# Performance work log

Hardware: AMD Instinct MI355X
Metric: run time of the kernel (lower is better)

## Reference

```python
import jax, jax.numpy as jnp
import numpy as np

TAU = 2.0       # LIF time constant
ALPHA = 4.0     # spikingjelly Sigmoid surrogate alpha
EPS = 1e-5      # BatchNorm eps
NUM_HEADS = 8

@jax.custom_vjp
def _spike(x):
    return (x >= 0.0).astype(x.dtype)

def _spike_fwd(x):
    return _spike(x), x

def _spike_bwd(x, g):
    s = jax.nn.sigmoid(ALPHA * x)
    return (g * ALPHA * s * (1.0 - s),)

_spike.defvjp(_spike_fwd, _spike_bwd)

def lif(x, v_th=1.0):
    """Multi-step LIF over leading time axis. v <- v + (x - v)/tau; hard reset to 0.
    detach_reset=True: spike in reset path is stop-gradient'ed."""
    def step(v, xt):
        v = v + (xt - v) / TAU
        s = _spike(v - v_th)
        v = v * (1.0 - jax.lax.stop_gradient(s))
        return v, s
    _, out = jax.lax.scan(step, jnp.zeros_like(x[0]), x)
    return out

def conv_bn(x, w, gamma, beta, mean, var, bias=None):
    """1x1 Conv1d over channel dim + BatchNorm1d (inference-style, running stats).
    x: [T,B,C,N], w: [Cout,Cin]."""
    y = jnp.einsum('tbcn,dc->tbdn', x, w)
    if bias is not None:
        y = y + bias[None, None, :, None]
    inv = gamma * jax.lax.rsqrt(var + EPS)
    return (y - mean[None, None, :, None]) * inv[None, None, :, None] + beta[None, None, :, None]

def _bn_params(key, C):
    k1, k2, k3 = jax.random.split(key, 3)
    gamma = 1.0 + 0.1 * jax.random.normal(k1, (C,), jnp.float32)
    beta = 0.1 * jax.random.normal(k2, (C,), jnp.float32)
    mean = 0.1 * jax.random.normal(k3, (C,), jnp.float32)
    var = jnp.ones((C,), jnp.float32)
    return gamma, beta, mean, var

def setup_inputs() -> dict:
    key = jax.random.key(0)
    ks = jax.random.split(key, 10)
    T, B, C, N = 4, 8, 512, 1024
    scale = 1.0 / np.sqrt(C)
    d = {}
    d['q'] = jax.random.normal(ks[0], (T, B, C, N), jnp.float32)
    d['k'] = jax.random.normal(ks[1], (T, B, C, N), jnp.float32)
    d['q_w'] = jax.random.normal(ks[2], (C, C), jnp.float32) * scale
    d['k_w'] = jax.random.normal(ks[3], (C, C), jnp.float32) * scale
    d['proj_w'] = jax.random.normal(ks[4], (C, C), jnp.float32) * scale
    d['proj_b'] = 0.01 * jax.random.normal(ks[5], (C,), jnp.float32)
    d['q_gamma'], d['q_beta'], d['q_mean'], d['q_var'] = _bn_params(ks[6], C)
    d['k_gamma'], d['k_beta'], d['k_mean'], d['k_var'] = _bn_params(ks[7], C)
    d['proj_gamma'], d['proj_beta'], d['proj_mean'], d['proj_var'] = _bn_params(ks[8], C)
    return d

def reference(q, k, q_w, k_w, proj_w, proj_b,
              q_gamma, q_beta, q_mean, q_var,
              k_gamma, k_beta, k_mean, k_var,
              proj_gamma, proj_beta, proj_mean, proj_var):
    T, B, C, N = q.shape
    H = NUM_HEADS
    Dh = C // H
    # Q path: conv1x1 + BN + LIF spikes, split heads
    q_s = lif(conv_bn(q, q_w, q_gamma, q_beta, q_mean, q_var))          # [T,B,C,N]
    q_h = q_s.reshape(T, B, H, Dh, N)
    # K path
    k_s = lif(conv_bn(k, k_w, k_gamma, k_beta, k_mean, k_var))          # [T,B,C,N]
    k_h = k_s.reshape(T, B, H, Dh, N)
    # Sum-pool Q over head_dim, spike-gate (threshold 0.5), multiply into K
    q_sum = jnp.sum(q_h, axis=3, keepdims=True)                         # [T,B,H,1,N]
    attn = lif(q_sum, v_th=0.5)                                         # [T,B,H,1,N]
    x = (attn * k_h).reshape(T, B, C, N)
    # Projection: conv1x1 (with bias) + BN + LIF
    x = conv_bn(x, proj_w, proj_gamma, proj_beta, proj_mean, proj_var, bias=proj_b)
    return lif(x)
```

## Files before the change

kernel.cpp:

```cpp
#include <hip/hip_runtime.h>
#include <hip/hip_fp16.h>
#include <stdint.h>

#define TT 4
#define BB 8
#define CC 512
#define NN 1024
#define HH 8

typedef unsigned char u8;
typedef _Float16 f16x8 __attribute__((ext_vector_type(8)));
typedef float f32x16 __attribute__((ext_vector_type(16)));

#define WF_BYTES ((size_t)2*64*512*16)
#define SZ_SPIKE ((size_t)TT*BB*CC*NN)
#define SZ_GATE  ((size_t)TT*BB*HH*NN)

union U4H { uint4 u; f16x8 v; };
__device__ __forceinline__ f16x8 ash(uint4 u){ U4H x; x.u = u; return x.v; }

#define MFMA_F16(a,b,c) __builtin_amdgcn_mfma_f32_32x32x16_f16((a),(b),(c),0,0,0)

__device__ __forceinline__ void gld_lds4(const void* g, void* l){
  __builtin_amdgcn_global_load_lds((const __attribute__((address_space(1))) void*)g,
                                   (__attribute__((address_space(3))) void*)l, 4, 0, 0);
}

#define WAITVM(N) asm volatile("s_waitcnt vmcnt(" #N ")" ::: "memory")
#define WAITLGKM0 asm volatile("s_waitcnt lgkmcnt(0)" ::: "memory")
#define SBAR() __builtin_amdgcn_s_barrier()
#define VMFENCE() asm volatile("" ::: "memory")

__device__ __forceinline__ void split16(float xs, uint32_t& h, uint32_t& m){
  __half hh = __float2half(xs);
  float hf = __half2float(hh);
  __half mm = __float2half(xs - hf);
  h = __half_as_ushort(hh);
  m = __half_as_ushort(mm);
}

__global__ __launch_bounds__(256)
void k_prep(const float* __restrict__ W0, const float* __restrict__ W1,
            const float* __restrict__ W2,
            u8* __restrict__ D0, u8* __restrict__ D1, u8* __restrict__ D2)
{
  const int which = blockIdx.y;
  const float* W = (which == 0) ? W0 : (which == 1) ? W1 : W2;
  u8* D = (which == 0) ? D0 : (which == 1) ? D1 : D2;
  const int tg  = blockIdx.x * 256 + threadIdx.x;
  const int row = tg >> 6;
  const int kh  = tg & 63;
  uint32_t Hw[4], Mw[4];
#pragma unroll
  for (int p = 0; p < 4; ++p){
    uint32_t h0, m0, h1, m1;
    split16(W[row * CC + kh * 8 + 2*p    ] * 64.0f, h0, m0);
    split16(W[row * CC + kh * 8 + 2*p + 1] * 64.0f, h1, m1);
    Hw[p] = h0 | (h1 << 16);
    Mw[p] = m0 | (m1 << 16);
  }
  *(uint4*)(D + ((size_t)(0*64 + kh)*512 + row) * 16) = make_uint4(Hw[0],Hw[1],Hw[2],Hw[3]);
  *(uint4*)(D + ((size_t)(1*64 + kh)*512 + row) * 16) = make_uint4(Mw[0],Mw[1],Mw[2],Mw[3]);
}

__global__ __launch_bounds__(512, 2)
void k_qk(const float* __restrict__ Q, const float* __restrict__ K,
          const u8* __restrict__ WFq, const u8* __restrict__ WFk,
          const float* __restrict__ qg, const float* __restrict__ qb,
          const float* __restrict__ qm, const float* __restrict__ qv,
          const float* __restrict__ kg, const float* __restrict__ kb,
          const float* __restrict__ km, const float* __restrict__ kv,
          u8* __restrict__ Sk, u8* __restrict__ Aa)
{
  __shared__ uint4 frag[2][1024];

  const int hw = blockIdx.x;
  const int lg = (hw & 7) * 64 + (hw >> 3);
  const int n0i  = lg & 31;
  const int b    = (lg >> 5) & 7;
  const int path = (lg >> 8) & 1;
  const int n0 = n0i << 5;
  const float* X = path ? K : Q;
  const u8* WF = path ? WFk : WFq;

  const int tid = threadIdx.x, lane = tid & 63, wid = tid >> 6;
  const int hi = lane >> 5, ln31 = lane & 31;

  const int c  = tid & 127;
  const int kq = tid >> 7;
  const int ct_t = c >> 5, nn = c & 31;
  const float* Xb = X + ((size_t)(ct_t*BB + b)*CC)*NN + n0 + nn;

  f32x16 acc[4][2];
#pragma unroll
  for (int i = 0; i < 4; ++i)
#pragma unroll
    for (int j = 0; j < 2; ++j)
#pragma unroll
      for (int r = 0; r < 16; ++r) acc[i][j][r] = 0.0f;

  uint4 A0[8], A1[8];
  float xr[8];

  auto loadX = [&](int tile){
    const float* xp = Xb + (size_t)(tile*32 + kq*8)*NN;
#pragma unroll
    for (int j = 0; j < 8; ++j) xr[j] = xp[(size_t)j*NN];
  };
  auto loadA = [&](int H, uint4* A){
#pragma unroll
    for (int s = 0; s < 2; ++s)
#pragma unroll
      for (int ksc = 0; ksc < 2; ++ksc)
#pragma unroll
        for (int rt = 0; rt < 2; ++rt)
          A[(s*2 + ksc)*2 + rt] = *(const uint4*)(WF +
              ((size_t)(s*64 + H*4 + ksc*2 + hi)*512
               + wid*64 + rt*32 + ln31) * 16);
  };
  auto split_write = [&](int fb){
    uint32_t hw_[4], mw_[4];
#pragma unroll
    for (int p = 0; p < 4; ++p){
      uint32_t ha, ma, hb2, mb2;
      split16(xr[2*p    ] * 512.0f, ha, ma);
      split16(xr[2*p + 1] * 512.0f, hb2, mb2);
      hw_[p] = ha | (hb2 << 16);
      mw_[p] = ma | (mb2 << 16);
    }
    frag[fb][      kq*128 + c] = make_uint4(hw_[0],hw_[1],hw_[2],hw_[3]);
    frag[fb][(4 + kq)*128 + c] = make_uint4(mw_[0],mw_[1],mw_[2],mw_[3]);
  };
  auto mstep = [&](const uint4* A, int fb){
#pragma unroll
    for (int ksc = 0; ksc < 2; ++ksc){
      const int klr = ksc*2 + hi;
#pragma unroll
      for (int ct = 0; ct < 4; ++ct){
        f16x8 bh = ash(frag[fb][klr*128 + ct*32 + ln31]);
        f16x8 bm = ash(frag[fb][(4 + klr)*128 + ct*32 + ln31]);
#pragma unroll
        for (int rt = 0; rt < 2; ++rt){
          acc[ct][rt] = MFMA_F16(ash(A[(0*2 + ksc)*2 + rt]), bh, acc[ct][rt]);
          acc[ct][rt] = MFMA_F16(ash(A[(1*2 + ksc)*2 + rt]), bh, acc[ct][rt]);
          acc[ct][rt] = MFMA_F16(ash(A[(0*2 + ksc)*2 + rt]), bm, acc[ct][rt]);
        }
      }
    }
  };

  loadX(0); VMFENCE();
  loadA(0, A0); VMFENCE();
  WAITVM(8);
  split_write(0);
  loadX(1); VMFENCE();
  WAITLGKM0; SBAR();

#define QK_IT(H, AC, AN) { \
    loadA((H)+1, AN); VMFENCE(); \
    WAITVM(16); \
    mstep(AC, (H)&1); \
    WAITVM(8); \
    split_write(((H)+1)&1); \
    if ((H) < 14) { loadX((H)+2); VMFENCE(); } \
    WAITLGKM0; SBAR(); }

  QK_IT(0,  A0, A1)  QK_IT(1,  A1, A0)
  QK_IT(2,  A0, A1)  QK_IT(3,  A1, A0)
  QK_IT(4,  A0, A1)  QK_IT(5,  A1, A0)
  QK_IT(6,  A0, A1)  QK_IT(7,  A1, A0)
  QK_IT(8,  A0, A1)  QK_IT(9,  A1, A0)
  QK_IT(10, A0, A1)  QK_IT(11, A1, A0)
  QK_IT(12, A0, A1)  QK_IT(13, A1, A0)
  QK_IT(14, A0, A1)
  { WAITVM(0); mstep(A1, 1); }
#undef QK_IT

  const float* gamma = path ? kg : qg;
  const float* beta  = path ? kb : qb;
  const float* mean  = path ? km : qm;
  const float* var   = path ? kv : qv;

  uint32_t orb = 0;
#pragma unroll
  for (int rt = 0; rt < 2; ++rt)
#pragma unroll
    for (int rg = 0; rg < 4; ++rg){
      const int dbase = wid*64 + rt*32 + rg*8 + hi*4;
      const float4 g4 = *(const float4*)&gamma[dbase];
      const float4 b4 = *(const float4*)&beta[dbase];
      const float4 m4 = *(const float4*)&mean[dbase];
      const float4 v4 = *(const float4*)&var[dbase];
      const float* gp = (const float*)&g4;
      const float* bp = (const float*)&b4;
      const float* mp = (const float*)&m4;
      const float* vp = (const float*)&v4;
#pragma unroll
      for (int j = 0; j < 4; ++j){
        const float inv = gp[j] * (1.0f / sqrtf(vp[j] + 1e-5f));
        const float c1 = inv * (1.0f/32768.0f);
        const float c0 = bp[j] - mp[j]*inv;
        const int r = rg*4 + j;
        float v = 0.f;
#pragma unroll
        for (int t = 0; t < 4; ++t){
          const float y = fmaf(acc[t][rt][r], c1, c0);
          v = 0.5f*(v + y);
          const bool s = (v >= 1.0f);
          if (s) v = 0.f;
          if (path == 1)
            Sk[((size_t)(t*BB + b)*CC + dbase + j)*NN + n0 + ln31] = (u8)s;
          else
            orb |= ((uint32_t)s) << t;
        }
      }
    }

  if (path == 0){
    orb |= __shfl_xor(orb, 32);
    if (hi == 0){
#pragma unroll
      for (int t = 0; t < 4; ++t)
        Aa[((size_t)(t*BB + b)*HH + wid)*NN + n0 + ln31] = (u8)((orb >> t) & 1);
    }
  }
}

__global__ __launch_bounds__(256, 2)
void k_proj(const u8* __restrict__ Sk, const u8* __restrict__ Ag,
            const u8* __restrict__ WF, const float* __restrict__ bias,
            const float* __restrict__ gamma, const float* __restrict__ beta,
            const float* __restrict__ mean, const float* __restrict__ var,
            float* __restrict__ O)
{
  __shared__ u8   xu[3][8192];
  __shared__ uint4 frag[1024];

  const int hw = blockIdx.x;
  const int lg = (hw & 7) * 64 + (hw >> 3);
  const int d0t = lg & 1;
  const int n0i = (lg >> 1) & 31;
  const int b   = (lg >> 6) & 7;
  const int n0 = n0i << 5, d0 = d0t << 8;

  const int tid = threadIdx.x, lane = tid & 63, wid = tid >> 6;
  const int hi = lane >> 5, ln31 = lane & 31;

  const int st_kh = tid >> 5, st_t = (tid >> 3) & 3, st_n4 = tid & 7;

  f32x16 acc[4][2];
#pragma unroll
  for (int t = 0; t < 4; ++t)
#pragma unroll
    for (int rt = 0; rt < 2; ++rt)
#pragma unroll
      for (int r = 0; r < 16; ++r) acc[t][rt][r] = 0.0f;

  uint4 Ap[16];
  uint32_t gword[8];
#pragma unroll
  for (int p = 0; p < 8; ++p)
    gword[p] = *(const uint32_t*)(Ag +
        ((size_t)(st_t*BB + b)*HH + p)*NN + n0 + st_n4*4);

  auto xustage = [&](int h, int buf){
#pragma unroll
    for (int i = 0; i < 8; ++i){
      const u8* g = Sk + ((size_t)((wid*BB + b)*CC) + (size_t)(h*64 + i*8 + (lane >> 3)))*NN
                       + n0 + (lane & 7)*4;
      gld_lds4(g, (void*)&xu[buf][(wid*64 + i*8)*32]);
    }
  };
  auto loadPA = [&](int p){
#pragma unroll
    for (int s = 0; s < 2; ++s)
#pragma unroll
      for (int ks = 0; ks < 4; ++ks)
#pragma unroll
        for (int rt = 0; rt < 2; ++rt)
          Ap[(s*4 + ks)*2 + rt] = *(const uint4*)(WF +
              ((size_t)(s*64 + p*8 + ks*2 + hi)*512
               + d0 + wid*64 + rt*32 + ln31) * 16);
  };
  auto stage2 = [&](int buf, uint32_t g32){
    uint32_t r[8];
#pragma unroll
    for (int cc = 0; cc < 8; ++cc)
      r[cc] = *(const uint32_t*)&xu[buf][(st_t*64 + st_kh*8 + cc)*32 + st_n4*4];
#pragma unroll
    for (int j = 0; j < 4; ++j){
      const uint32_t gm   = __builtin_amdgcn_perm(g32, g32, (uint32_t)j * 0x01010101u);
      const uint32_t selp = (uint32_t)j | (((uint32_t)j + 4u) << 8);
      uint32_t p01 = __builtin_amdgcn_perm(r[1], r[0], selp);
      uint32_t p23 = __builtin_amdgcn_perm(r[3], r[2], selp);
      uint32_t p45 = __builtin_amdgcn_perm(r[5], r[4], selp);
      uint32_t p67 = __builtin_amdgcn_perm(r[7], r[6], selp);
      uint32_t lo  = __builtin_amdgcn_perm(p23, p01, 0x05040100u) & gm;
      uint32_t hi_ = __builtin_amdgcn_perm(p67, p45, 0x05040100u) & gm;
      uint32_t w[4];
#pragma unroll
      for (int p = 0; p < 4; ++p){
        const uint32_t src = (p < 2) ? lo : hi_;
        const uint32_t b0 = (src >> ((p & 1) * 16)) & 0xFFu;
        const uint32_t b1 = (src >> ((p & 1) * 16 + 8)) & 0xFFu;
        w[p] = (b0 ? 0x3C00u : 0u) | (b1 ? 0x3C000000u : 0u);
      }
      frag[st_kh*128 + st_t*32 + st_n4*4 + j] = make_uint4(w[0], w[1], w[2], w[3]);
    }
  };
  auto mstepP = [&](){
#pragma unroll
    for (int ks = 0; ks < 4; ++ks){
      const int kbi = ks*2 + hi;
#pragma unroll
      for (int ct = 0; ct < 4; ++ct){
        const int fb = ct*32 + ln31;
        f16x8 bb = ash(frag[kbi*128 + fb]);
#pragma unroll
        for (int rt = 0; rt < 2; ++rt){
          acc[ct][rt] = MFMA_F16(ash(Ap[(0*4 + ks)*2 + rt]), bb, acc[ct][rt]);
          acc[ct][rt] = MFMA_F16(ash(Ap[(1*4 + ks)*2 + rt]), bb, acc[ct][rt]);
        }
      }
    }
  };

#define PJ_PH(P, VM) { \
    WAITVM(VM); SBAR(); \
    loadPA(P); VMFENCE(); \
    if ((P) < 6) { xustage((P)+2, ((P)+2)%3); VMFENCE(); } \
    stage2((P)%3, gword[P]); \
    WAITLGKM0; SBAR(); \
    mstepP(); }

  xustage(0, 0); VMFENCE(); xustage(1, 1); VMFENCE();
  PJ_PH(0,8) PJ_PH(1,8) PJ_PH(2,8) PJ_PH(3,8)
  PJ_PH(4,8) PJ_PH(5,8) PJ_PH(6,8) PJ_PH(7,0)
#undef PJ_PH

#pragma unroll
  for (int rt = 0; rt < 2; ++rt)
#pragma unroll
    for (int rg = 0; rg < 4; ++rg){
      const int dbase = d0 + wid*64 + rt*32 + rg*8 + hi*4;
      const float4 g4 = *(const float4*)&gamma[dbase];
      const float4 b4 = *(const float4*)&beta[dbase];
      const float4 m4 = *(const float4*)&mean[dbase];
      const float4 v4 = *(const float4*)&var[dbase];
      const float4 s4 = *(const float4*)&bias[dbase];
      const float* gp = (const float*)&g4;
      const float* bp = (const float*)&b4;
      const float* mp = (const float*)&m4;
      const float* vp = (const float*)&v4;
      const float* sp = (const float*)&s4;
#pragma unroll
      for (int j = 0; j < 4; ++j){
        const float inv = gp[j] * (1.0f / sqrtf(vp[j] + 1e-5f));
        const float c1 = inv * (1.0f/64.0f);
        const float c0 = (sp[j] - mp[j])*inv + bp[j];
        const int r = rg*4 + j;
        float v = 0.f;
#pragma unroll
        for (int t = 0; t < 4; ++t){
          const float y = fmaf(acc[t][rt][r], c1, c0);
          v = 0.5f*(v + y);
          const bool s = (v >= 1.0f);
          if (s) v = 0.f;
          O[((size_t)(t*BB + b)*CC + dbase + j)*NN + n0 + ln31] = s ? 1.f : 0.f;
        }
      }
    }
}

extern "C" void kernel_launch(void* const* d_in, const int* in_sizes, int n_in,
                              void* d_out, int out_size, void* d_ws, size_t ws_size,
                              hipStream_t stream)
{
  const float* q   = (const float*)d_in[0];
  const float* k   = (const float*)d_in[1];
  const float* qw  = (const float*)d_in[2];
  const float* kw  = (const float*)d_in[3];
  const float* pw  = (const float*)d_in[4];
  const float* pb  = (const float*)d_in[5];
  const float* qg  = (const float*)d_in[6];
  const float* qbt = (const float*)d_in[7];
  const float* qm  = (const float*)d_in[8];
  const float* qv  = (const float*)d_in[9];
  const float* kg  = (const float*)d_in[10];
  const float* kbt = (const float*)d_in[11];
  const float* km  = (const float*)d_in[12];
  const float* kv  = (const float*)d_in[13];
  const float* pg  = (const float*)d_in[14];
  const float* pbt = (const float*)d_in[15];
  const float* pm  = (const float*)d_in[16];
  const float* pv  = (const float*)d_in[17];

  u8* WFq = (u8*)d_ws;
  u8* WFk = WFq + WF_BYTES;
  u8* WFp = WFk + WF_BYTES;
  u8* Sk  = WFp + WF_BYTES;
  u8* Aa  = Sk + SZ_SPIKE;
  const size_t need = 3*WF_BYTES + SZ_SPIKE + SZ_GATE;
  if (ws_size < need) return;

  k_prep<<<dim3(128, 3), 256, 0, stream>>>(qw, kw, pw, WFq, WFk, WFp);
  k_qk<<<512, 512, 0, stream>>>(q, k, WFq, WFk,
                                qg, qbt, qm, qv, kg, kbt, km, kv, Sk, Aa);
  k_proj<<<512, 256, 0, stream>>>(Sk, Aa, WFp, pb, pg, pbt, pm, pv, (float*)d_out);
}
```

Measured before the change: 158.8 us.

## Double k_qk block to 1024 threads with one row-tile per wave

The QK conv kernel now runs 1024 threads per block, and each of the 16 waves owns a single 32-row output tile instead of two. Per-thread accumulators, weight-fragment registers and X loads are halved, and the double-buffered A registers become a single buffer loaded after each MFMA step. Because a head now spans two waves, the Q-path head OR-reduction moves to LDS atomics followed by packed 32-bit stores. The goal is more waves resident to hide global-load latency, at the cost of losing the A-register prefetch overlap and adding extra barriers and atomics.

```diff
diff --git a/kernel.cpp b/kernel.cpp
--- a/kernel.cpp
+++ b/kernel.cpp
@@ -63,7 +63,7 @@
   *(uint4*)(D + ((size_t)(1*64 + kh)*512 + row) * 16) = make_uint4(Mw[0],Mw[1],Mw[2],Mw[3]);
 }
 
-__global__ __launch_bounds__(512, 2)
+__global__ __launch_bounds__(1024, 4)
 void k_qk(const float* __restrict__ Q, const float* __restrict__ K,
           const u8* __restrict__ WFq, const u8* __restrict__ WFk,
           const float* __restrict__ qg, const float* __restrict__ qb,
@@ -91,47 +91,41 @@
   const int ct_t = c >> 5, nn = c & 31;
   const float* Xb = X + ((size_t)(ct_t*BB + b)*CC)*NN + n0 + nn;
 
-  f32x16 acc[4][2];
+  f32x16 acc[4];
 #pragma unroll
   for (int i = 0; i < 4; ++i)
 #pragma unroll
-    for (int j = 0; j < 2; ++j)
-#pragma unroll
-      for (int r = 0; r < 16; ++r) acc[i][j][r] = 0.0f;
-
-  uint4 A0[8], A1[8];
-  float xr[8];
+    for (int r = 0; r < 16; ++r) acc[i][r] = 0.0f;
+
+  uint4 A[4];
+  float xr[4];
 
   auto loadX = [&](int tile){
-    const float* xp = Xb + (size_t)(tile*32 + kq*8)*NN;
-#pragma unroll
-    for (int j = 0; j < 8; ++j) xr[j] = xp[(size_t)j*NN];
-  };
-  auto loadA = [&](int H, uint4* A){
+    const float* xp = Xb + (size_t)(tile*32 + kq*4)*NN;
+#pragma unroll
+    for (int j = 0; j < 4; ++j) xr[j] = xp[(size_t)j*NN];
+  };
+  auto loadA = [&](int H){
 #pragma unroll
     for (int s = 0; s < 2; ++s)
 #pragma unroll
       for (int ksc = 0; ksc < 2; ++ksc)
-#pragma unroll
-        for (int rt = 0; rt < 2; ++rt)
-          A[(s*2 + ksc)*2 + rt] = *(const uint4*)(WF +
-              ((size_t)(s*64 + H*4 + ksc*2 + hi)*512
-               + wid*64 + rt*32 + ln31) * 16);
+        A[s*2 + ksc] = *(const uint4*)(WF +
+            ((size_t)(s*64 + H*4 + ksc*2 + hi)*512 + wid*32 + ln31) * 16);
   };
   auto split_write = [&](int fb){
-    uint32_t hw_[4], mw_[4];
-#pragma unroll
-    for (int p = 0; p < 4; ++p){
-      uint32_t ha, ma, hb2, mb2;
-      split16(xr[2*p    ] * 512.0f, ha, ma);
-      split16(xr[2*p + 1] * 512.0f, hb2, mb2);
-      hw_[p] = ha | (hb2 << 16);
-      mw_[p] = ma | (mb2 << 16);
-    }
-    frag[fb][      kq*128 + c] = make_uint4(hw_[0],hw_[1],hw_[2],hw_[3]);
-    frag[fb][(4 + kq)*128 + c] = make_uint4(mw_[0],mw_[1],mw_[2],mw_[3]);
-  };
-  auto mstep = [&](const uint4* A, int fb){
+    uint32_t h0,m0,h1,m1,h2,m2,h3,m3;
+    split16(xr[0] * 512.0f, h0, m0);
+    split16(xr[1] * 512.0f, h1, m1);
+    split16(xr[2] * 512.0f, h2, m2);
+    split16(xr[3] * 512.0f, h3, m3);
+    const uint2 hw_ = make_uint2(h0 | (h1 << 16), h2 | (h3 << 16));
+    const uint2 mw_ = make_uint2(m0 | (m1 << 16), m2 | (m3 << 16));
+    const int row = kq >> 1, half = kq & 1;
+    *((uint2*)&frag[fb][row*128 + c] + half)       = hw_;
+    *((uint2*)&frag[fb][(4 + row)*128 + c] + half) = mw_;
+  };
+  auto mstep = [&](int fb){
 #pragma unroll
     for (int ksc = 0; ksc < 2; ++ksc){
       const int klr = ksc*2 + hi;
@@ -139,41 +133,32 @@
       for (int ct = 0; ct < 4; ++ct){
         f16x8 bh = ash(frag[fb][klr*128 + ct*32 + ln31]);
         f16x8 bm = ash(frag[fb][(4 + klr)*128 + ct*32 + ln31]);
-#pragma unroll
-        for (int rt = 0; rt < 2; ++rt){
-          acc[ct][rt] = MFMA_F16(ash(A[(0*2 + ksc)*2 + rt]), bh, acc[ct][rt]);
-          acc[ct][rt] = MFMA_F16(ash(A[(1*2 + ksc)*2 + rt]), bh, acc[ct][rt]);
-          acc[ct][rt] = MFMA_F16(ash(A[(0*2 + ksc)*2 + rt]), bm, acc[ct][rt]);
-        }
+        acc[ct] = MFMA_F16(ash(A[0*2 + ksc]), bh, acc[ct]);
+        acc[ct] = MFMA_F16(ash(A[1*2 + ksc]), bh, acc[ct]);
+        acc[ct] = MFMA_F16(ash(A[0*2 + ksc]), bm, acc[ct]);
       }
     }
   };
 
   loadX(0); VMFENCE();
-  loadA(0, A0); VMFENCE();
-  WAITVM(8);
+  WAITVM(0);
   split_write(0);
   loadX(1); VMFENCE();
+  loadA(0); VMFENCE();
   WAITLGKM0; SBAR();
 
-#define QK_IT(H, AC, AN) { \
-    loadA((H)+1, AN); VMFENCE(); \
-    WAITVM(16); \
-    mstep(AC, (H)&1); \
-    WAITVM(8); \
-    split_write(((H)+1)&1); \
+#define QK_IT(H) { \
+    WAITVM(4); \
+    if ((H) < 15) split_write(((H)+1)&1); \
     if ((H) < 14) { loadX((H)+2); VMFENCE(); } \
+    mstep((H)&1); \
+    if ((H) < 15) { loadA((H)+1); VMFENCE(); } \
     WAITLGKM0; SBAR(); }
 
-  QK_IT(0,  A0, A1)  QK_IT(1,  A1, A0)
-  QK_IT(2,  A0, A1)  QK_IT(3,  A1, A0)
-  QK_IT(4,  A0, A1)  QK_IT(5,  A1, A0)
-  QK_IT(6,  A0, A1)  QK_IT(7,  A1, A0)
-  QK_IT(8,  A0, A1)  QK_IT(9,  A1, A0)
-  QK_IT(10, A0, A1)  QK_IT(11, A1, A0)
-  QK_IT(12, A0, A1)  QK_IT(13, A1, A0)
-  QK_IT(14, A0, A1)
-  { WAITVM(0); mstep(A1, 1); }
+  QK_IT(0)  QK_IT(1)  QK_IT(2)  QK_IT(3)
+  QK_IT(4)  QK_IT(5)  QK_IT(6)  QK_IT(7)
+  QK_IT(8)  QK_IT(9)  QK_IT(10) QK_IT(11)
+  QK_IT(12) QK_IT(13) QK_IT(14) QK_IT(15)
 #undef QK_IT
 
   const float* gamma = path ? kg : qg;
@@ -183,45 +168,52 @@
 
   uint32_t orb = 0;
 #pragma unroll
-  for (int rt = 0; rt < 2; ++rt)
-#pragma unroll
-    for (int rg = 0; rg < 4; ++rg){
-      const int dbase = wid*64 + rt*32 + rg*8 + hi*4;
-      const float4 g4 = *(const float4*)&gamma[dbase];
-      const float4 b4 = *(const float4*)&beta[dbase];
-      const float4 m4 = *(const float4*)&mean[dbase];
-      const float4 v4 = *(const float4*)&var[dbase];
-      const float* gp = (const float*)&g4;
-      const float* bp = (const float*)&b4;
-      const float* mp = (const float*)&m4;
-      const float* vp = (const float*)&v4;
-#pragma unroll
-      for (int j = 0; j < 4; ++j){
-        const float inv = gp[j] * (1.0f / sqrtf(vp[j] + 1e-5f));
-        const float c1 = inv * (1.0f/32768.0f);
-        const float c0 = bp[j] - mp[j]*inv;
-        const int r = rg*4 + j;
-        float v = 0.f;
-#pragma unroll
-        for (int t = 0; t < 4; ++t){
-          const float y = fmaf(acc[t][rt][r], c1, c0);
-          v = 0.5f*(v + y);
-          const bool s = (v >= 1.0f);
-          if (s) v = 0.f;
-          if (path == 1)
-            Sk[((size_t)(t*BB + b)*CC + dbase + j)*NN + n0 + ln31] = (u8)s;
-          else
-            orb |= ((uint32_t)s) << t;
-        }
+  for (int rg = 0; rg < 4; ++rg){
+    const int dbase = wid*32 + rg*8 + hi*4;
+    const float4 g4 = *(const float4*)&gamma[dbase];
+    const float4 b4 = *(const float4*)&beta[dbase];
+    const float4 m4 = *(const float4*)&mean[dbase];
+    const float4 v4 = *(const float4*)&var[dbase];
+    const float* gp = (const float*)&g4;
+    const float* bp = (const float*)&b4;
+    const float* mp = (const float*)&m4;
+    const float* vp = (const float*)&v4;
+#pragma unroll
+    for (int j = 0; j < 4; ++j){
+      const float inv = gp[j] * (1.0f / sqrtf(vp[j] + 1e-5f));
+      const float c1 = inv * (1.0f/32768.0f);
+      const float c0 = bp[j] - mp[j]*inv;
+      const int r = rg*4 + j;
+      float v = 0.f;
+#pragma unroll
+      for (int t = 0; t < 4; ++t){
+        const float y = fmaf(acc[t][r], c1, c0);
+        v = 0.5f*(v + y);
+        const bool s = (v >= 1.0f);
+        if (s) v = 0.f;
+        if (path == 1)
+          Sk[((size_t)(t*BB + b)*CC + dbase + j)*NN + n0 + ln31] = (u8)s;
+        else
+          orb |= ((uint32_t)s) << t;
       }
     }
+  }
 
   if (path == 0){
-    orb |= __shfl_xor(orb, 32);
-    if (hi == 0){
-#pragma unroll
-      for (int t = 0; t < 4; ++t)
-        Aa[((size_t)(t*BB + b)*HH + wid)*NN + n0 + ln31] = (u8)((orb >> t) & 1);
+    __syncthreads();
+    uint32_t* gw = (uint32_t*)&frag[0][0];
+    if (tid < 256) gw[tid] = 0;
+    __syncthreads();
+    const int head = wid >> 1;
+#pragma unroll
+    for (int t = 0; t < 4; ++t)
+      if ((orb >> t) & 1)
+        atomicOr(&gw[head*32 + t*8 + (ln31 >> 2)], 1u << ((ln31 & 3)*8));
+    __syncthreads();
+    if (tid < 256){
+      const int h = tid >> 5, t = (tid >> 3) & 3, nw = tid & 7;
+      *(uint32_t*)(Aa + ((size_t)(t*BB + b)*HH + h)*NN + n0 + nw*4) =
+          gw[h*32 + t*8 + nw];
     }
   }
 }
@@ -404,7 +396,7 @@
   if (ws_size < need) return;
 
   k_prep<<<dim3(128, 3), 256, 0, stream>>>(qw, kw, pw, WFq, WFk, WFp);
-  k_qk<<<512, 512, 0, stream>>>(q, k, WFq, WFk,
-                                qg, qbt, qm, qv, kg, kbt, km, kv, Sk, Aa);
+  k_qk<<<512, 1024, 0, stream>>>(q, k, WFq, WFk,
+                                 qg, qbt, qm, qv, kg, kbt, km, kv, Sk, Aa);
   k_proj<<<512, 256, 0, stream>>>(Sk, Aa, WFp, pb, pg, pbt, pm, pv, (float*)d_out);
 }
```

Measured after the change: 157.1 us. About the same (-1.1%).

## Deepen k_qk K-tile to 64 with per-phase weight prefetch and MFMA priority

Applied to the files above, without the earlier changes.

The Q/K projection kernel now processes 64 input channels per barrier step instead of 32, so the main loop has 8 stages rather than 16. Shared memory for the activation fragments doubles to match. Weight fragments are split into four phase buffers, and each buffer is refilled for the next tile right after its MFMA phase consumes it. MFMA phases also raise wave priority with s_setprio. The aims are fewer block barriers and finer-grained overlap of weight loads with compute, at the cost of more registers for the 16 activation values and more LDS per block, which could reduce occupancy.

```diff
diff --git a/kernel.cpp b/kernel.cpp
--- a/kernel.cpp
+++ b/kernel.cpp
@@ -72,7 +72,7 @@
           const float* __restrict__ km, const float* __restrict__ kv,
           u8* __restrict__ Sk, u8* __restrict__ Aa)
 {
-  __shared__ uint4 frag[2][1024];
+  __shared__ uint4 frag[2][2048];
 
   const int hw = blockIdx.x;
   const int lg = (hw & 7) * 64 + (hw >> 3);
@@ -99,82 +99,76 @@
 #pragma unroll
       for (int r = 0; r < 16; ++r) acc[i][j][r] = 0.0f;
 
-  uint4 A0[8], A1[8];
-  float xr[8];
+  uint4 A0[4], A1[4], A2[4], A3[4];
+  float xr[16];
 
   auto loadX = [&](int tile){
-    const float* xp = Xb + (size_t)(tile*32 + kq*8)*NN;
-#pragma unroll
-    for (int j = 0; j < 8; ++j) xr[j] = xp[(size_t)j*NN];
-  };
-  auto loadA = [&](int H, uint4* A){
-#pragma unroll
-    for (int s = 0; s < 2; ++s)
-#pragma unroll
-      for (int ksc = 0; ksc < 2; ++ksc)
-#pragma unroll
-        for (int rt = 0; rt < 2; ++rt)
-          A[(s*2 + ksc)*2 + rt] = *(const uint4*)(WF +
-              ((size_t)(s*64 + H*4 + ksc*2 + hi)*512
-               + wid*64 + rt*32 + ln31) * 16);
+    const float* xp = Xb + (size_t)(tile*64 + kq*16)*NN;
+#pragma unroll
+    for (int j = 0; j < 16; ++j) xr[j] = xp[(size_t)j*NN];
   };
   auto split_write = [&](int fb){
-    uint32_t hw_[4], mw_[4];
-#pragma unroll
-    for (int p = 0; p < 4; ++p){
-      uint32_t ha, ma, hb2, mb2;
-      split16(xr[2*p    ] * 512.0f, ha, ma);
-      split16(xr[2*p + 1] * 512.0f, hb2, mb2);
-      hw_[p] = ha | (hb2 << 16);
-      mw_[p] = ma | (mb2 << 16);
-    }
-    frag[fb][      kq*128 + c] = make_uint4(hw_[0],hw_[1],hw_[2],hw_[3]);
-    frag[fb][(4 + kq)*128 + c] = make_uint4(mw_[0],mw_[1],mw_[2],mw_[3]);
-  };
-  auto mstep = [&](const uint4* A, int fb){
-#pragma unroll
-    for (int ksc = 0; ksc < 2; ++ksc){
-      const int klr = ksc*2 + hi;
-#pragma unroll
-      for (int ct = 0; ct < 4; ++ct){
-        f16x8 bh = ash(frag[fb][klr*128 + ct*32 + ln31]);
-        f16x8 bm = ash(frag[fb][(4 + klr)*128 + ct*32 + ln31]);
-#pragma unroll
-        for (int rt = 0; rt < 2; ++rt){
-          acc[ct][rt] = MFMA_F16(ash(A[(0*2 + ksc)*2 + rt]), bh, acc[ct][rt]);
-          acc[ct][rt] = MFMA_F16(ash(A[(1*2 + ksc)*2 + rt]), bh, acc[ct][rt]);
-          acc[ct][rt] = MFMA_F16(ash(A[(0*2 + ksc)*2 + rt]), bm, acc[ct][rt]);
-        }
+#pragma unroll
+    for (int half = 0; half < 2; ++half){
+      uint32_t hw_[4], mw_[4];
+#pragma unroll
+      for (int p = 0; p < 4; ++p){
+        uint32_t ha, ma, hb2, mb2;
+        split16(xr[half*8 + 2*p    ] * 512.0f, ha, ma);
+        split16(xr[half*8 + 2*p + 1] * 512.0f, hb2, mb2);
+        hw_[p] = ha | (hb2 << 16);
+        mw_[p] = ma | (mb2 << 16);
       }
-    }
-  };
+      const int oct = kq*2 + half;
+      frag[fb][      oct*128 + c] = make_uint4(hw_[0],hw_[1],hw_[2],hw_[3]);
+      frag[fb][(8 + oct)*128 + c] = make_uint4(mw_[0],mw_[1],mw_[2],mw_[3]);
+    }
+  };
+
+#define LOADA(T, PH, A_) { \
+    _Pragma("unroll") \
+    for (int s = 0; s < 2; ++s) \
+      _Pragma("unroll") \
+      for (int rt = 0; rt < 2; ++rt) \
+        A_[s*2 + rt] = *(const uint4*)(WF + \
+            ((size_t)(s*64 + (T)*8 + (PH)*2 + hi)*512 \
+             + wid*64 + rt*32 + ln31) * 16); }
+
+#define MPHASE(FB, KS, A_) { \
+    const int oct_ = (KS)*2 + hi; \
+    __builtin_amdgcn_s_setprio(1); \
+    _Pragma("unroll") \
+    for (int ct = 0; ct < 4; ++ct){ \
+      f16x8 bh = ash(frag[FB][      oct_*128 + ct*32 + ln31]); \
+      f16x8 bm = ash(frag[FB][(8 + oct_)*128 + ct*32 + ln31]); \
+      _Pragma("unroll") \
+      for (int rt = 0; rt < 2; ++rt){ \
+        acc[ct][rt] = MFMA_F16(ash(A_[0*2 + rt]), bh, acc[ct][rt]);  \
+        acc[ct][rt] = MFMA_F16(ash(A_[1*2 + rt]), bh, acc[ct][rt]);  \
+        acc[ct][rt] = MFMA_F16(ash(A_[0*2 + rt]), bm, acc[ct][rt]);  \
+      } } \
+    __builtin_amdgcn_s_setprio(0); }
 
   loadX(0); VMFENCE();
-  loadA(0, A0); VMFENCE();
-  WAITVM(8);
+  WAITVM(0);
   split_write(0);
   loadX(1); VMFENCE();
+  LOADA(0,0,A0) LOADA(0,1,A1) LOADA(0,2,A2) LOADA(0,3,A3) VMFENCE();
   WAITLGKM0; SBAR();
 
-#define QK_IT(H, AC, AN) { \
-    loadA((H)+1, AN); VMFENCE(); \
-    WAITVM(16); \
-    mstep(AC, (H)&1); \
-    WAITVM(8); \
-    split_write(((H)+1)&1); \
-    if ((H) < 14) { loadX((H)+2); VMFENCE(); } \
-    WAITLGKM0; SBAR(); }
-
-  QK_IT(0,  A0, A1)  QK_IT(1,  A1, A0)
-  QK_IT(2,  A0, A1)  QK_IT(3,  A1, A0)
-  QK_IT(4,  A0, A1)  QK_IT(5,  A1, A0)
-  QK_IT(6,  A0, A1)  QK_IT(7,  A1, A0)
-  QK_IT(8,  A0, A1)  QK_IT(9,  A1, A0)
-  QK_IT(10, A0, A1)  QK_IT(11, A1, A0)
-  QK_IT(12, A0, A1)  QK_IT(13, A1, A0)
-  QK_IT(14, A0, A1)
-  { WAITVM(0); mstep(A1, 1); }
-#undef QK_IT
+#define QK_T(T) { \
+    if ((T) >= 1 && (T) <= 6) { loadX((T)+1); VMFENCE(); } \
+    MPHASE((T)&1, 0, A0)  if ((T) < 7) { LOADA((T)+1, 0, A0) VMFENCE(); } \
+    MPHASE((T)&1, 1, A1)  if ((T) < 7) { LOADA((T)+1, 1, A1) VMFENCE(); } \
+    MPHASE((T)&1, 2, A2)  if ((T) < 7) { LOADA((T)+1, 2, A2) VMFENCE(); } \
+    MPHASE((T)&1, 3, A3)  if ((T) < 7) { LOADA((T)+1, 3, A3) VMFENCE(); \
+      WAITVM(16); split_write(((T)+1)&1); WAITLGKM0; SBAR(); } }
+
+  QK_T(0) QK_T(1) QK_T(2) QK_T(3)
+  QK_T(4) QK_T(5) QK_T(6) QK_T(7)
+#undef QK_T
+#undef MPHASE
+#undef LOADA
 
   const float* gamma = path ? kg : qg;
   const float* beta  = path ? kb : qb;
```

After: 157.1 us (median of 2 runs). About the same (-1.1%).

## Split QK GEMM over output-channel quarters with LDS-staged LIF epilogue

Applied to the files above, without the earlier changes.

k_qk now gives each block 128 output channels instead of all 512, so the launch grows from 512 to 2048 blocks. Each wave holds only two accumulators, and the launch-bounds occupancy target rises to 4 blocks per CU. The A-fragment loads are split into two phases per K tile, with MFMA priority raised around the compute. The epilogue stages accumulators through a shared-memory transpose so the LIF and spike writes use a cleaner thread mapping, and the gate bits are built with shared atomicOr. The trade-off is that each X tile is now loaded and split four times, once per channel quarter, and the 64KB LDS union may cap occupancy below the requested 4.

```diff
diff --git a/kernel.cpp b/kernel.cpp
--- a/kernel.cpp
+++ b/kernel.cpp
@@ -63,7 +63,7 @@
   *(uint4*)(D + ((size_t)(1*64 + kh)*512 + row) * 16) = make_uint4(Mw[0],Mw[1],Mw[2],Mw[3]);
 }
 
-__global__ __launch_bounds__(512, 2)
+__global__ __launch_bounds__(512, 4)
 void k_qk(const float* __restrict__ Q, const float* __restrict__ K,
           const u8* __restrict__ WFq, const u8* __restrict__ WFk,
           const float* __restrict__ qg, const float* __restrict__ qb,
@@ -72,34 +72,38 @@
           const float* __restrict__ km, const float* __restrict__ kv,
           u8* __restrict__ Sk, u8* __restrict__ Aa)
 {
-  __shared__ uint4 frag[2][1024];
+  __shared__ union {
+    uint4 frag[2][1024];
+    float y[128*128];
+  } Lds;
+  __shared__ uint32_t gw[64];
 
   const int hw = blockIdx.x;
-  const int lg = (hw & 7) * 64 + (hw >> 3);
-  const int n0i  = lg & 31;
-  const int b    = (lg >> 5) & 7;
-  const int path = (lg >> 8) & 1;
-  const int n0 = n0i << 5;
+  const int lg = (hw & 7) * 256 + (hw >> 3);
+  const int d0q  = lg & 3;
+  const int n0i  = (lg >> 2) & 31;
+  const int b    = (lg >> 7) & 7;
+  const int path = (lg >> 10) & 1;
+  const int n0 = n0i << 5, d0 = d0q << 7;
   const float* X = path ? K : Q;
   const u8* WF = path ? WFk : WFq;
 
   const int tid = threadIdx.x, lane = tid & 63, wid = tid >> 6;
   const int hi = lane >> 5, ln31 = lane & 31;
+  const int wd = wid >> 2, wc = wid & 3;
 
   const int c  = tid & 127;
   const int kq = tid >> 7;
   const int ct_t = c >> 5, nn = c & 31;
   const float* Xb = X + ((size_t)(ct_t*BB + b)*CC)*NN + n0 + nn;
 
-  f32x16 acc[4][2];
-#pragma unroll
-  for (int i = 0; i < 4; ++i)
-#pragma unroll
-    for (int j = 0; j < 2; ++j)
-#pragma unroll
-      for (int r = 0; r < 16; ++r) acc[i][j][r] = 0.0f;
-
-  uint4 A0[8], A1[8];
+  f32x16 acc[2];
+#pragma unroll
+  for (int i = 0; i < 2; ++i)
+#pragma unroll
+    for (int r = 0; r < 16; ++r) acc[i][r] = 0.0f;
+
+  uint4 A0_[4], A1_[4];
   float xr[8];
 
   auto loadX = [&](int tile){
@@ -107,18 +111,19 @@
 #pragma unroll
     for (int j = 0; j < 8; ++j) xr[j] = xp[(size_t)j*NN];
   };
-  auto loadA = [&](int H, uint4* A){
+  auto loadA = [&](int H, int ksc, uint4* A_){
 #pragma unroll
     for (int s = 0; s < 2; ++s)
 #pragma unroll
-      for (int ksc = 0; ksc < 2; ++ksc)
-#pragma unroll
-        for (int rt = 0; rt < 2; ++rt)
-          A[(s*2 + ksc)*2 + rt] = *(const uint4*)(WF +
-              ((size_t)(s*64 + H*4 + ksc*2 + hi)*512
-               + wid*64 + rt*32 + ln31) * 16);
+      for (int rd = 0; rd < 2; ++rd)
+        A_[s*2 + rd] = *(const uint4*)(WF +
+            ((size_t)(s*64 + H*4 + ksc*2 + hi)*512
+             + d0 + wd*64 + rd*32 + ln31) * 16);
   };
   auto split_write = [&](int fb){
+#pragma unroll
+    for (int half = 0; half < 2; ++half){
+    }
     uint32_t hw_[4], mw_[4];
 #pragma unroll
     for (int p = 0; p < 4; ++p){
@@ -128,100 +133,106 @@
       hw_[p] = ha | (hb2 << 16);
       mw_[p] = ma | (mb2 << 16);
     }
-    frag[fb][      kq*128 + c] = make_uint4(hw_[0],hw_[1],hw_[2],hw_[3]);
-    frag[fb][(4 + kq)*128 + c] = make_uint4(mw_[0],mw_[1],mw_[2],mw_[3]);
-  };
-  auto mstep = [&](const uint4* A, int fb){
-#pragma unroll
-    for (int ksc = 0; ksc < 2; ++ksc){
-      const int klr = ksc*2 + hi;
-#pragma unroll
-      for (int ct = 0; ct < 4; ++ct){
-        f16x8 bh = ash(frag[fb][klr*128 + ct*32 + ln31]);
-        f16x8 bm = ash(frag[fb][(4 + klr)*128 + ct*32 + ln31]);
-#pragma unroll
-        for (int rt = 0; rt < 2; ++rt){
-          acc[ct][rt] = MFMA_F16(ash(A[(0*2 + ksc)*2 + rt]), bh, acc[ct][rt]);
-          acc[ct][rt] = MFMA_F16(ash(A[(1*2 + ksc)*2 + rt]), bh, acc[ct][rt]);
-          acc[ct][rt] = MFMA_F16(ash(A[(0*2 + ksc)*2 + rt]), bm, acc[ct][rt]);
-        }
-      }
-    }
+    Lds.frag[fb][      kq*128 + c] = make_uint4(hw_[0],hw_[1],hw_[2],hw_[3]);
+    Lds.frag[fb][(4 + kq)*128 + c] = make_uint4(mw_[0],mw_[1],mw_[2],mw_[3]);
+  };
+  auto mstep_ph = [&](int fb, int ksc, const uint4* A_){
+    const int klr = ksc*2 + hi;
+    f16x8 bh = ash(Lds.frag[fb][      klr*128 + wc*32 + ln31]);
+    f16x8 bm = ash(Lds.frag[fb][(4 + klr)*128 + wc*32 + ln31]);
+    __builtin_amdgcn_s_setprio(1);
+#pragma unroll
+    for (int rd = 0; rd < 2; ++rd){
+      acc[rd] = MFMA_F16(ash(A_[0*2 + rd]), bh, acc[rd]);
+      acc[rd] = MFMA_F16(ash(A_[1*2 + rd]), bh, acc[rd]);
+      acc[rd] = MFMA_F16(ash(A_[0*2 + rd]), bm, acc[rd]);
+    }
+    __builtin_amdgcn_s_setprio(0);
   };
 
   loadX(0); VMFENCE();
-  loadA(0, A0); VMFENCE();
-  WAITVM(8);
+  WAITVM(0);
   split_write(0);
+  loadA(0, 0, A0_); VMFENCE();
+  loadA(0, 1, A1_); VMFENCE();
   loadX(1); VMFENCE();
   WAITLGKM0; SBAR();
 
-#define QK_IT(H, AC, AN) { \
-    loadA((H)+1, AN); VMFENCE(); \
-    WAITVM(16); \
-    mstep(AC, (H)&1); \
-    WAITVM(8); \
-    split_write(((H)+1)&1); \
-    if ((H) < 14) { loadX((H)+2); VMFENCE(); } \
-    WAITLGKM0; SBAR(); }
-
-  QK_IT(0,  A0, A1)  QK_IT(1,  A1, A0)
-  QK_IT(2,  A0, A1)  QK_IT(3,  A1, A0)
-  QK_IT(4,  A0, A1)  QK_IT(5,  A1, A0)
-  QK_IT(6,  A0, A1)  QK_IT(7,  A1, A0)
-  QK_IT(8,  A0, A1)  QK_IT(9,  A1, A0)
-  QK_IT(10, A0, A1)  QK_IT(11, A1, A0)
-  QK_IT(12, A0, A1)  QK_IT(13, A1, A0)
-  QK_IT(14, A0, A1)
-  { WAITVM(0); mstep(A1, 1); }
+#define QK_IT(H) { \
+    WAITVM(12); \
+    mstep_ph((H)&1, 0, A0_); \
+    if ((H) < 15) { loadA((H)+1, 0, A0_); VMFENCE(); } \
+    WAITVM(12); \
+    mstep_ph((H)&1, 1, A1_); \
+    if ((H) < 15) { \
+      loadA((H)+1, 1, A1_); VMFENCE(); \
+      WAITVM(8); \
+      split_write(((H)+1)&1); \
+      if ((H) < 14) { loadX((H)+2); VMFENCE(); } \
+      WAITLGKM0; SBAR(); \
+    } }
+
+  QK_IT(0)  QK_IT(1)  QK_IT(2)  QK_IT(3)
+  QK_IT(4)  QK_IT(5)  QK_IT(6)  QK_IT(7)
+  QK_IT(8)  QK_IT(9)  QK_IT(10) QK_IT(11)
+  QK_IT(12) QK_IT(13) QK_IT(14) QK_IT(15)
 #undef QK_IT
+
+  if (path == 0 && tid < 64) gw[tid] = 0;
+  __syncthreads();
+  {
+    const int colb = wc*32 + ln31;
+#pragma unroll
+    for (int rd = 0; rd < 2; ++rd)
+#pragma unroll
+      for (int r = 0; r < 16; ++r){
+        const int row = wd*64 + rd*32 + (r & 3) + ((r >> 2) << 3) + (hi << 2);
+        Lds.y[row*128 + colb] = acc[rd][r];
+      }
+  }
+  __syncthreads();
 
   const float* gamma = path ? kg : qg;
   const float* beta  = path ? kb : qb;
   const float* mean  = path ? km : qm;
   const float* var   = path ? kv : qv;
 
-  uint32_t orb = 0;
-#pragma unroll
-  for (int rt = 0; rt < 2; ++rt)
-#pragma unroll
-    for (int rg = 0; rg < 4; ++rg){
-      const int dbase = wid*64 + rt*32 + rg*8 + hi*4;
-      const float4 g4 = *(const float4*)&gamma[dbase];
-      const float4 b4 = *(const float4*)&beta[dbase];
-      const float4 m4 = *(const float4*)&mean[dbase];
-      const float4 v4 = *(const float4*)&var[dbase];
-      const float* gp = (const float*)&g4;
-      const float* bp = (const float*)&b4;
-      const float* mp = (const float*)&m4;
-      const float* vp = (const float*)&v4;
-#pragma unroll
-      for (int j = 0; j < 4; ++j){
-        const float inv = gp[j] * (1.0f / sqrtf(vp[j] + 1e-5f));
-        const float c1 = inv * (1.0f/32768.0f);
-        const float c0 = bp[j] - mp[j]*inv;
-        const int r = rg*4 + j;
-        float v = 0.f;
-#pragma unroll
-        for (int t = 0; t < 4; ++t){
-          const float y = fmaf(acc[t][rt][r], c1, c0);
-          v = 0.5f*(v + y);
-          const bool s = (v >= 1.0f);
-          if (s) v = 0.f;
-          if (path == 1)
-            Sk[((size_t)(t*BB + b)*CC + dbase + j)*NN + n0 + ln31] = (u8)s;
-          else
-            orb |= ((uint32_t)s) << t;
-        }
-      }
-    }
+  const int nn_e = tid & 31, dl = tid >> 5;
+#pragma unroll
+  for (int i = 0; i < 8; ++i){
+    const int d = i*16 + dl;
+    const int dg = d0 + d;
+    const float inv = gamma[dg] * (1.0f / sqrtf(var[dg] + 1e-5f));
+    const float c1 = inv * (1.0f/32768.0f);
+    const float c0 = beta[dg] - mean[dg]*inv;
+    float v = 0.f;
+    uint32_t sb = 0;
+#pragma unroll
+    for (int t = 0; t < 4; ++t){
+      const float y = fmaf(Lds.y[d*128 + t*32 + nn_e], c1, c0);
+      v = 0.5f*(v + y);
+      const bool s = (v >= 1.0f);
+      if (s) v = 0.f;
+      if (path == 1)
+        Sk[((size_t)(t*BB + b)*CC + dg)*NN + n0 + nn_e] = (u8)s;
+      else
+        sb |= ((uint32_t)s) << t;
+    }
+    if (path == 0 && sb){
+      const int hl = d >> 6;
+#pragma unroll
+      for (int t = 0; t < 4; ++t)
+        if ((sb >> t) & 1)
+          atomicOr(&gw[hl*32 + t*8 + (nn_e >> 2)], 1u << ((nn_e & 3)*8));
+    }
+  }
 
   if (path == 0){
-    orb |= __shfl_xor(orb, 32);
-    if (hi == 0){
-#pragma unroll
-      for (int t = 0; t < 4; ++t)
-        Aa[((size_t)(t*BB + b)*HH + wid)*NN + n0 + ln31] = (u8)((orb >> t) & 1);
+    __syncthreads();
+    if (tid < 64){
+      const int hl = tid >> 5, t = (tid >> 3) & 3, nw = tid & 7;
+      *(uint32_t*)(Aa + ((size_t)(t*BB + b)*HH + (d0 >> 6) + hl)*NN + n0 + nw*4) =
+          gw[hl*32 + t*8 + nw];
     }
   }
 }
@@ -404,7 +415,7 @@
   if (ws_size < need) return;
 
   k_prep<<<dim3(128, 3), 256, 0, stream>>>(qw, kw, pw, WFq, WFk, WFp);
-  k_qk<<<512, 512, 0, stream>>>(q, k, WFq, WFk,
-                                qg, qbt, qm, qv, kg, kbt, km, kv, Sk, Aa);
+  k_qk<<<2048, 512, 0, stream>>>(q, k, WFq, WFk,
+                                 qg, qbt, qm, qv, kg, kbt, km, kv, Sk, Aa);
   k_proj<<<512, 256, 0, stream>>>(Sk, Aa, WFp, pb, pg, pbt, pm, pv, (float*)d_out);
 }
```

Measured after the change: 191.9 us. 1.21x slower.
